# Kernel tuning notes

Measured on AMD Instinct MI355X. Metric: run time of the kernel, lower is better.

## Reference

```python
import jax, jax.numpy as jnp
import numpy as np

B, S, A, H, N = 4096, 128, 32, 1024, 256
BETA = 1.0            # params['temperature']
NORM_SMOOTHING = 0.01 # params['norm_smoothing']
MAX_A = 1.0           # env.action_space.high[0]
# dropout_rate = 0.0 and eval-mode reference -> dropout is identity


def setup_inputs() -> dict:
    key = jax.random.key(0)
    ks = jax.random.split(key, 16)
    sc_s = 1.0 / np.sqrt(S)
    sc_h = 1.0 / np.sqrt(H)
    return {
        "s": jax.random.normal(ks[0], (B, S), jnp.float32),
        "a": jax.random.normal(ks[1], (B, A), jnp.float32),
        # value side MLP: S->H->H->H->N
        "Wv1": jax.random.uniform(ks[2], (S, H), jnp.float32, -sc_s, sc_s),
        "bv1": jax.random.uniform(ks[3], (H,), jnp.float32, -sc_s, sc_s),
        "Wv2": jax.random.uniform(ks[4], (H, H), jnp.float32, -sc_h, sc_h),
        "bv2": jax.random.uniform(ks[5], (H,), jnp.float32, -sc_h, sc_h),
        "Wv3": jax.random.uniform(ks[6], (H, H), jnp.float32, -sc_h, sc_h),
        "bv3": jax.random.uniform(ks[7], (H,), jnp.float32, -sc_h, sc_h),
        "Wv4": jax.random.uniform(ks[8], (H, N), jnp.float32, -sc_h, sc_h),
        "bv4": jax.random.uniform(ks[9], (N,), jnp.float32, -sc_h, sc_h),
        # location side: S->H (xavier), then N expert linears H->A stacked
        "Wl1": jax.random.normal(ks[10], (S, H), jnp.float32) * np.sqrt(2.0 / (S + H)),
        "bl1": jnp.zeros((H,), jnp.float32),
        "Wexp": jax.random.uniform(ks[11], (N, H, A), jnp.float32, -0.1, 0.1),
        "bexp": jax.random.uniform(ks[12], (N, A), jnp.float32, -1.0, 1.0),
    }


def reference(s, a, Wv1, bv1, Wv2, bv2, Wv3, bv3, Wv4, bv4, Wl1, bl1, Wexp, bexp):
    t = jax.nn.relu(s @ Wv1 + bv1)
    t = jax.nn.relu(t @ Wv2 + bv2)
    t = jax.nn.relu(t @ Wv3 + bv3)
    values = t @ Wv4 + bv4                      # [B, N]

    # --- get_all_centroids: shared hidden, N expert heads as grouped GEMM ---
    h = jax.nn.relu(s @ Wl1 + bl1)              # [B, H] (dropout identity)
    centroids = MAX_A * jnp.tanh(
        jnp.einsum("bh,nha->bna", h, Wexp) + bexp[None]
    )                                           # [B, N, A]

    # --- rbf_function: softmax over -beta * ||centroid - a|| ---
    diff = centroids - a[:, None, :]            # [B, N, A]
    dist = jnp.sqrt(jnp.sum(diff * diff, axis=2) + NORM_SMOOTHING)  # [B, N]
    weights = jax.nn.softmax(-BETA * dist, axis=1)                  # [B, N]

    return jnp.sum(weights * values, axis=1, keepdims=True)         # [B, 1]
```

## Files before the change

### kernel.cpp

```cpp
#include <hip/hip_runtime.h>
#include <hip/hip_bf16.h>


typedef _Float16 half8 __attribute__((ext_vector_type(8)));
typedef _Float16 half4v __attribute__((ext_vector_type(4)));
typedef float floatx16 __attribute__((ext_vector_type(16)));

namespace {
constexpr int kB = 4096, kS = 128, kA = 32, kH = 1024, kN = 256;
constexpr size_t al(size_t x) { return (x + 255) & ~size_t(255); }
constexpr size_t OFF_FLAG  = 0;
constexpr size_t OFF_S16   = 256;
constexpr size_t OFF_WEXPT = OFF_S16   + al((size_t)kB * kS * 2);
constexpr size_t OFF_WV1T  = OFF_WEXPT + al((size_t)kN * kA * kH * 2);
constexpr size_t OFF_WL1T  = OFF_WV1T  + (size_t)kS * kH * 2;
constexpr size_t OFF_WV2T  = OFF_WL1T  + al((size_t)kS * kH * 2);
constexpr size_t OFF_WV3T  = OFF_WV2T  + al((size_t)kH * kH * 2);
constexpr size_t OFF_WV4T  = OFF_WV3T  + al((size_t)kH * kH * 2);
constexpr size_t OFF_BUFC  = OFF_WV4T  + al((size_t)kH * kN * 2);
constexpr size_t OFF_B2V   = OFF_BUFC  + al((size_t)kB * 2 * kH * 2);
constexpr size_t OFF_B3    = OFF_B2V   + al((size_t)kB * kH * 2);
constexpr size_t OFF_VAL   = OFF_B3    + al((size_t)kB * kH * 2);
constexpr size_t OFF_DIST  = OFF_VAL   + al((size_t)kB * kN * 4);
}

__device__ __forceinline__ float ldraw(const void* p, size_t i, int bf) {
    if (bf) return __uint_as_float(((unsigned)((const unsigned short*)p)[i]) << 16);
    return ((const float*)p)[i];
}

__device__ __forceinline__ float4 ldraw4(const void* p, size_t i, int bf) {
    if (bf) {
        ushort4 u = *(const ushort4*)((const unsigned short*)p + i);
        return make_float4(__uint_as_float((unsigned)u.x << 16),
                           __uint_as_float((unsigned)u.y << 16),
                           __uint_as_float((unsigned)u.z << 16),
                           __uint_as_float((unsigned)u.w << 16));
    }
    return *(const float4*)((const float*)p + i);
}

__device__ __forceinline__ void gl_lds16(const _Float16* g, _Float16* l) {
    __builtin_amdgcn_global_load_lds(
        (const __attribute__((address_space(1))) unsigned int*)g,
        (__attribute__((address_space(3))) unsigned int*)l, 16, 0, 0);
}

template <int N>
__device__ __forceinline__ void waitcnt_vm() {
    if constexpr (N == 0)      asm volatile("s_waitcnt vmcnt(0)" ::: "memory");
    else if constexpr (N == 2) asm volatile("s_waitcnt vmcnt(2)" ::: "memory");
    else if constexpr (N == 4) asm volatile("s_waitcnt vmcnt(4)" ::: "memory");
    else if constexpr (N == 6) asm volatile("s_waitcnt vmcnt(6)" ::: "memory");
    else if constexpr (N == 8) asm volatile("s_waitcnt vmcnt(8)" ::: "memory");
    else if constexpr (N == 16) asm volatile("s_waitcnt vmcnt(16)" ::: "memory");
    else static_assert(N == 0, "unsupported vmcnt");
}

__device__ __forceinline__ float fast_tanh(float x) {
    x = fminf(9.f, fmaxf(-9.f, x));
    float e = __expf(2.f * x);
    return (e - 1.f) * __builtin_amdgcn_rcpf(e + 1.f);
}

__global__ void detect_kernel(const unsigned int* __restrict__ s_raw, int* __restrict__ flag) {
    __shared__ int cnt;
    if (threadIdx.x == 0) cnt = 0;
    __syncthreads();
    const unsigned e = (s_raw[threadIdx.x] >> 7) & 0xFFu;
    int c = (e >= 118u && e <= 135u) ? 1 : 0;
    for (int off = 32; off > 0; off >>= 1) c += __shfl_down(c, off);
    if ((threadIdx.x & 63) == 0) atomicAdd(&cnt, c);
    __syncthreads();
    if (threadIdx.x == 0) *flag = (cnt > 128) ? 1 : 0;
}

struct TDesc { const void* src; _Float16* dst; int K; int N; int tiles; };
struct TPack { TDesc d[7]; };

__global__ void transpose_all(TPack p, const int* __restrict__ flag) {
    __shared__ float tile[32][33];
    const int bf = *flag;
    int bid = blockIdx.x;
    int i = 0;
    while (bid >= p.d[i].tiles) { bid -= p.d[i].tiles; ++i; }
    const void* src = p.d[i].src;
    _Float16* dst = p.d[i].dst;
    const int tx = threadIdx.x, ty = threadIdx.y;
    const int K = p.d[i].K, N = p.d[i].N;
    if (K == 0) {
        const int lin = ty * 8 + tx;
        const size_t base = (size_t)bid * 4096;
#pragma unroll
        for (int t = 0; t < 4; ++t) {
            const size_t idx = base + (size_t)t * 1024 + (size_t)lin * 4;
            float4 v = ldraw4(src, idx, bf);
            half4v o = {(_Float16)v.x, (_Float16)v.y, (_Float16)v.z, (_Float16)v.w};
            *(half4v*)(dst + idx) = o;
        }
        return;
    }
    const int tpz = (N >> 5) * (K >> 5);
    const int z = bid / tpz, r = bid - z * tpz;
    const int n0 = (r % (N >> 5)) * 32, k0 = (r / (N >> 5)) * 32;
    const size_t zo = (size_t)z * K * N;
    float4 v = ldraw4(src, zo + (size_t)(k0 + ty) * N + n0 + tx * 4, bf);
    tile[ty][tx * 4 + 0] = v.x;
    tile[ty][tx * 4 + 1] = v.y;
    tile[ty][tx * 4 + 2] = v.z;
    tile[ty][tx * 4 + 3] = v.w;
    __syncthreads();
    half4v o;
#pragma unroll
    for (int j = 0; j < 4; ++j) o[j] = (_Float16)tile[tx * 4 + j][ty];
    *(half4v*)(dst + zo + (size_t)(n0 + ty) * K + k0 + tx * 4) = o;
}

struct GArgs {
    const _Float16* A;
    const _Float16* Bt;
    const void* bias;
    const void* bias2;
    void* C;
    const void* a_raw;
    float* dist;
    int split;
    int N, K, lda, Mt, Nt, relu, of16, fuse;
};

template <int TM, int TN, int WM, int WN, int NST>
__device__ __forceinline__ void dgemm_core(const GArgs& g, int bid, const int* flagp) {
    constexpr int NT = WM * WN * 64;
    constexpr int BK = 32;
    constexpr int MI = TM / WM / 32, NI = TN / WN / 32;
    constexpr int ACH = TM * BK / 8;
    constexpr int BCH = TN * BK / 8;
    constexpr int AT = (ACH + NT - 1) / NT;
    constexpr int BT = (BCH + NT - 1) / NT;
    constexpr int LPS = AT + BT;
    __shared__ _Float16 As[NST * ACH * 8];
    __shared__ _Float16 Bs[NST * BCH * 8];

    const int tid = threadIdx.x;
    const int lane = tid & 63;
    const int w = tid >> 6, wr = w / WN, wc = w % WN;
    const int N = g.N, K = g.K, lda = g.lda;

    int mt, nt;
    if ((g.Mt & 7) == 0 && (g.Nt & 7) == 0) {
        const int xcd = bid & 7, loc = bid >> 3;
        const int Bn = g.Nt >> 3;
        const int sr = loc / (8 * Bn);
        const int rem = loc - sr * (8 * Bn);
        mt = sr * 8 + (rem & 7);
        nt = xcd * Bn + (rem >> 3);
    } else {
        mt = bid % g.Mt;
        nt = bid / g.Mt;
    }
    const int m0 = mt * TM, n0 = nt * TN;

    const _Float16* gAsrc[AT];
    _Float16* lAdst[AT];
#pragma unroll
    for (int t = 0; t < AT; ++t) {
        int c = t * NT + tid;
        if (c >= ACH) c = ACH - 1;
        const int ks = c / (TM * 2), rem = c % (TM * 2);
        const int row = (rem >> 6) * 32 + (rem & 31);
        const int kcol = ks * 16 + ((rem >> 5) & 1) * 8;
        gAsrc[t] = g.A + (size_t)(m0 + row) * lda + kcol;
        lAdst[t] = As + c * 8;
    }
    const _Float16* gBsrc[BT];
    _Float16* lBdst[BT];
#pragma unroll
    for (int t = 0; t < BT; ++t) {
        int c = t * NT + tid;
        if (c >= BCH) c = BCH - 1;
        const int ks = c / (TN * 2), rem = c % (TN * 2);
        const int row = (rem >> 6) * 32 + (rem & 31);
        const int kcol = ks * 16 + ((rem >> 5) & 1) * 8;
        gBsrc[t] = g.Bt + (size_t)(n0 + row) * K + kcol;
        lBdst[t] = Bs + c * 8;
    }

    auto issue = [&](int k0, int st) {
#pragma unroll
        for (int t = 0; t < AT; ++t)
            if ((t + 1) * NT <= ACH || t * NT + tid < ACH)
                gl_lds16(gAsrc[t] + k0, lAdst[t] + st * ACH * 8);
#pragma unroll
        for (int t = 0; t < BT; ++t)
            if ((t + 1) * NT <= BCH || t * NT + tid < BCH)
                gl_lds16(gBsrc[t] + k0, lBdst[t] + st * BCH * 8);
    };

    floatx16 acc[MI][NI];
#pragma unroll
    for (int mi = 0; mi < MI; ++mi)
#pragma unroll
        for (int ni = 0; ni < NI; ++ni)
#pragma unroll
            for (int i = 0; i < 16; ++i) acc[mi][ni][i] = 0.f;

    auto compute = [&](int st) {
        const int ao = st * ACH * 8, bo = st * BCH * 8;
#pragma unroll
        for (int ks = 0; ks < 2; ++ks) {
            half8 af[MI], bf[NI];
#pragma unroll
            for (int mi = 0; mi < MI; ++mi)
                af[mi] = *(const half8*)(As + ao + ((size_t)(ks * TM * 2 + (wr * MI + mi) * 64 + lane)) * 8);
#pragma unroll
            for (int ni = 0; ni < NI; ++ni)
                bf[ni] = *(const half8*)(Bs + bo + ((size_t)(ks * TN * 2 + (wc * NI + ni) * 64 + lane)) * 8);
#pragma unroll
            for (int mi = 0; mi < MI; ++mi)
#pragma unroll
                for (int ni = 0; ni < NI; ++ni)
                    acc[mi][ni] = __builtin_amdgcn_mfma_f32_32x32x16_f16(af[mi], bf[ni], acc[mi][ni], 0, 0, 0);
        }
    };

    const int ntiles = K / BK;
    if constexpr (NST == 2) {
        issue(0, 0);
        for (int k0 = 0; k0 < K; k0 += 2 * BK) {
            __syncthreads();
            if (k0 + BK < K) issue(k0 + BK, 1);
            compute(0);
            __syncthreads();
            if (k0 + 2 * BK < K) issue(k0 + 2 * BK, 0);
            compute(1);
        }
    } else {
        issue(0, 0);
        if (ntiles > 1) issue(BK, 1);
        if (ntiles > 2) issue(2 * BK, 2);
        for (int kt = 0; kt < ntiles; ++kt) {
            const int rem = ntiles - 1 - kt;
            if (rem >= 2)      waitcnt_vm<2 * LPS>();
            else if (rem == 1) waitcnt_vm<LPS>();
            else               waitcnt_vm<0>();
            __builtin_amdgcn_s_barrier();
            asm volatile("" ::: "memory");
            __builtin_amdgcn_sched_barrier(0);
            if (kt + 3 < ntiles) issue((kt + 3) * BK, (kt + 3) & 3);
            __builtin_amdgcn_s_setprio(1);
            compute(kt & 3);
            __builtin_amdgcn_s_setprio(0);
            asm volatile("s_waitcnt lgkmcnt(0)" ::: "memory");
        }
    }

    const int bf_ = *flagp;
    const int am = lane & 31;
    const int half = lane >> 5;

    if (g.fuse) {
        constexpr int EPB = TN / 32;
        const int ebase = n0 >> 5;
        float bvv[NI];
#pragma unroll
        for (int ni = 0; ni < NI; ++ni)
            bvv[ni] = ldraw(g.bias, (size_t)(n0 + (wc * NI + ni) * 32 + am), bf_);
        float* a_s = (float*)As;
        float* d_s = (float*)Bs;
        __syncthreads();
        for (int idx = tid; idx < TM * kA; idx += NT)
            a_s[idx] = ldraw(g.a_raw, (size_t)(m0 + (idx >> 5)) * kA + (idx & 31), bf_);
        __syncthreads();
#pragma unroll
        for (int mi = 0; mi < MI; ++mi)
#pragma unroll
            for (int rr = 0; rr < 16; ++rr) {
                const int row_loc = (wr * MI + mi) * 32 + (rr & 3) + 8 * (rr >> 2) + 4 * half;
                const float av = a_s[row_loc * kA + am];
#pragma unroll
                for (int ni = 0; ni < NI; ++ni) {
                    const float c = fast_tanh(acc[mi][ni][rr] + bvv[ni]);
                    const float d = c - av;
                    float d2 = d * d;
                    d2 += __shfl_xor(d2, 1);
                    d2 += __shfl_xor(d2, 2);
                    d2 += __shfl_xor(d2, 4);
                    d2 += __shfl_xor(d2, 8);
                    d2 += __shfl_xor(d2, 16);
                    if (am == 0) d_s[row_loc * EPB + wc * NI + ni] = d2;
                }
            }
        __syncthreads();
        for (int idx = tid; idx < TM * EPB; idx += NT)
            g.dist[(size_t)(m0 + (idx / EPB)) * kN + ebase + (idx % EPB)] = sqrtf(d_s[idx] + 0.01f);
        return;
    }

#pragma unroll
    for (int mi = 0; mi < MI; ++mi)
#pragma unroll
        for (int ni = 0; ni < NI; ++ni) {
            const int Rb = m0 + (wr * MI + mi) * 32;
            const int Cb = n0 + (wc * NI + ni) * 32 + am;
            const float bv = (Cb < g.split) ? ldraw(g.bias, Cb, bf_)
                                            : ldraw(g.bias2, Cb - g.split, bf_);
#pragma unroll
            for (int rr = 0; rr < 16; ++rr) {
                const int row = Rb + (rr & 3) + 8 * (rr >> 2) + 4 * half;
                float x = acc[mi][ni][rr] + bv;
                if (g.relu) x = fmaxf(x, 0.f);
                if (g.of16) ((_Float16*)g.C)[(size_t)row * N + Cb] = (_Float16)x;
                else ((float*)g.C)[(size_t)row * N + Cb] = x;
            }
        }
}

template <int TM, int TN, int WM, int WN, int NST, int MW>
__launch_bounds__(WM * WN * 64, MW)
__global__ void dgemm_one(GArgs g, const int* __restrict__ flagp) {
    dgemm_core<TM, TN, WM, WN, NST>(g, blockIdx.x, flagp);
}

__launch_bounds__(256)
__global__ void final_softmax(const float* __restrict__ dist, const float* __restrict__ values,
                              const int* __restrict__ flag, void* __restrict__ out) {
    const int row = blockIdx.x * 4 + (threadIdx.x >> 6);
    const int lane = threadIdx.x & 63;
    const float4 d4 = *(const float4*)(dist + (size_t)row * kN + lane * 4);
    const float4 v4 = *(const float4*)(values + (size_t)row * kN + lane * 4);
    float m = fminf(fminf(d4.x, d4.y), fminf(d4.z, d4.w));
#pragma unroll
    for (int off = 32; off > 0; off >>= 1) m = fminf(m, __shfl_xor(m, off));
    const float w0 = expf(m - d4.x), w1 = expf(m - d4.y);
    const float w2 = expf(m - d4.z), w3 = expf(m - d4.w);
    float ws = (w0 + w1) + (w2 + w3);
    float wv = fmaf(w0, v4.x, fmaf(w1, v4.y, fmaf(w2, v4.z, w3 * v4.w)));
#pragma unroll
    for (int off = 32; off > 0; off >>= 1) {
        ws += __shfl_xor(ws, off);
        wv += __shfl_xor(wv, off);
    }
    if (lane == 0) {
        const float o = wv / ws;
        if (*flag) ((__hip_bfloat16*)out)[row] = __float2bfloat16(o);
        else       ((float*)out)[row] = o;
    }
}

extern "C" void kernel_launch(void* const* d_in, const int* in_sizes, int n_in,
                              void* d_out, int out_size, void* d_ws, size_t ws_size,
                              hipStream_t stream) {
    (void)in_sizes; (void)n_in; (void)out_size; (void)ws_size;
    char* ws = (char*)d_ws;
    int* flag = (int*)(ws + OFF_FLAG);
    _Float16* s16   = (_Float16*)(ws + OFF_S16);
    _Float16* wexpt = (_Float16*)(ws + OFF_WEXPT);
    _Float16* wv1t  = (_Float16*)(ws + OFF_WV1T);
    _Float16* wl1t  = (_Float16*)(ws + OFF_WL1T);
    _Float16* wv2t  = (_Float16*)(ws + OFF_WV2T);
    _Float16* wv3t  = (_Float16*)(ws + OFF_WV3T);
    _Float16* wv4t  = (_Float16*)(ws + OFF_WV4T);
    _Float16* bufC  = (_Float16*)(ws + OFF_BUFC);
    _Float16* b2v   = (_Float16*)(ws + OFF_B2V);
    _Float16* b3    = (_Float16*)(ws + OFF_B3);
    float* values   = (float*)(ws + OFF_VAL);
    float* distb    = (float*)(ws + OFF_DIST);

    detect_kernel<<<1, 256, 0, stream>>>((const unsigned int*)d_in[0], flag);

    TPack tp;
    tp.d[0] = {d_in[2],  wv1t,  kS, kH, (kH / 32) * (kS / 32)};
    tp.d[1] = {d_in[10], wl1t,  kS, kH, (kH / 32) * (kS / 32)};
    tp.d[2] = {d_in[4],  wv2t,  kH, kH, (kH / 32) * (kH / 32)};
    tp.d[3] = {d_in[6],  wv3t,  kH, kH, (kH / 32) * (kH / 32)};
    tp.d[4] = {d_in[8],  wv4t,  kH, kN, (kN / 32) * (kH / 32)};
    tp.d[5] = {d_in[12], wexpt, kH, kA, kN * (kA / 32) * (kH / 32)};
    tp.d[6] = {d_in[0],  s16,   0,  kB * kS, (kB * kS) / 4096};
    int total_tiles = 0;
    for (int i = 0; i < 7; ++i) total_tiles += tp.d[i].tiles;
    transpose_all<<<total_tiles, dim3(8, 32), 0, stream>>>(tp, flag);

    const int BIG = 1 << 30;
    {
        GArgs g{s16, wv1t, d_in[3], d_in[11], bufC, nullptr, nullptr, kH,
                2 * kH, kS, kS, kB / 64, (2 * kH) / 64, 1, 1, 0};
        dgemm_one<64, 64, 2, 2, 4, 2><<<(kB / 64) * ((2 * kH) / 64), 256, 0, stream>>>(g, flag);
    }
    {
        GArgs g{bufC, wv2t, d_in[5], d_in[5], b2v, nullptr, nullptr, BIG,
                kH, kH, 2 * kH, kB / 128, kH / 128, 1, 1, 0};
        dgemm_one<128, 128, 2, 2, 4, 2><<<(kB / 128) * (kH / 128), 256, 0, stream>>>(g, flag);
    }
    {
        GArgs g{b2v, wv3t, d_in[7], d_in[7], b3, nullptr, nullptr, BIG,
                kH, kH, kH, kB / 128, kH / 128, 1, 1, 0};
        dgemm_one<128, 128, 2, 2, 4, 2><<<(kB / 128) * (kH / 128), 256, 0, stream>>>(g, flag);
    }
    {
        GArgs g{b3, wv4t, d_in[9], d_in[9], values, nullptr, nullptr, BIG,
                kN, kH, kH, kB / 64, kN / 64, 0, 0, 0};
        dgemm_one<64, 64, 2, 2, 4, 2><<<(kB / 64) * (kN / 64), 256, 0, stream>>>(g, flag);
    }
    {
        GArgs g{bufC + kH, wexpt, d_in[13], d_in[13], nullptr, d_in[1], distb,
                BIG, kN * kA, kH, 2 * kH, kB / 128, (kN * kA) / 128, 0, 0, 1};
        dgemm_one<128, 128, 2, 2, 2, 4><<<(kB / 128) * ((kN * kA) / 128), 256, 0, stream>>>(g, flag);
    }
    final_softmax<<<kB / 4, 256, 0, stream>>>(distb, values, flag, d_out);
}
```

Baseline: 358.5 us.

## Add dedicated 256x256 expert GEMM kernel with XCD-aware tile mapping

Moves the fused expert GEMM (tanh, distance and reduction epilogue) out of the generic templated kernel into a dedicated 512-thread kernel. The new kernel uses 256x256 tiles, a double-buffered BK=32 global-to-LDS pipeline, and a block-index remap that groups N-tiles per XCD. The aim is more operand reuse per tile and better L2 locality for the largest GEMM (4096x8192x1024). In exchange, the larger tile gives fewer blocks and shallower pipelining, and the fused path is removed from the generic kernel.

Result: faster. 350.2 us (-2.3%).

```diff
diff --git a/kernel.cpp b/kernel.cpp
--- a/kernel.cpp
+++ b/kernel.cpp
@@ -56,6 +56,7 @@
     else if constexpr (N == 16) asm volatile("s_waitcnt vmcnt(16)" ::: "memory");
     else static_assert(N == 0, "unsupported vmcnt");
 }
+__device__ __forceinline__ void lgkm0() { asm volatile("s_waitcnt lgkmcnt(0)" ::: "memory"); }
 
 __device__ __forceinline__ float fast_tanh(float x) {
     x = fminf(9.f, fmaxf(-9.f, x));
@@ -250,51 +251,13 @@
             __builtin_amdgcn_s_setprio(1);
             compute(kt & 3);
             __builtin_amdgcn_s_setprio(0);
-            asm volatile("s_waitcnt lgkmcnt(0)" ::: "memory");
+            lgkm0();
         }
     }
 
     const int bf_ = *flagp;
     const int am = lane & 31;
     const int half = lane >> 5;
-
-    if (g.fuse) {
-        constexpr int EPB = TN / 32;
-        const int ebase = n0 >> 5;
-        float bvv[NI];
-#pragma unroll
-        for (int ni = 0; ni < NI; ++ni)
-            bvv[ni] = ldraw(g.bias, (size_t)(n0 + (wc * NI + ni) * 32 + am), bf_);
-        float* a_s = (float*)As;
-        float* d_s = (float*)Bs;
-        __syncthreads();
-        for (int idx = tid; idx < TM * kA; idx += NT)
-            a_s[idx] = ldraw(g.a_raw, (size_t)(m0 + (idx >> 5)) * kA + (idx & 31), bf_);
-        __syncthreads();
-#pragma unroll
-        for (int mi = 0; mi < MI; ++mi)
-#pragma unroll
-            for (int rr = 0; rr < 16; ++rr) {
-                const int row_loc = (wr * MI + mi) * 32 + (rr & 3) + 8 * (rr >> 2) + 4 * half;
-                const float av = a_s[row_loc * kA + am];
-#pragma unroll
-                for (int ni = 0; ni < NI; ++ni) {
-                    const float c = fast_tanh(acc[mi][ni][rr] + bvv[ni]);
-                    const float d = c - av;
-                    float d2 = d * d;
-                    d2 += __shfl_xor(d2, 1);
-                    d2 += __shfl_xor(d2, 2);
-                    d2 += __shfl_xor(d2, 4);
-                    d2 += __shfl_xor(d2, 8);
-                    d2 += __shfl_xor(d2, 16);
-                    if (am == 0) d_s[row_loc * EPB + wc * NI + ni] = d2;
-                }
-            }
-        __syncthreads();
-        for (int idx = tid; idx < TM * EPB; idx += NT)
-            g.dist[(size_t)(m0 + (idx / EPB)) * kN + ebase + (idx % EPB)] = sqrtf(d_s[idx] + 0.01f);
-        return;
-    }
 
 #pragma unroll
     for (int mi = 0; mi < MI; ++mi)
@@ -319,6 +282,132 @@
 __launch_bounds__(WM * WN * 64, MW)
 __global__ void dgemm_one(GArgs g, const int* __restrict__ flagp) {
     dgemm_core<TM, TN, WM, WN, NST>(g, blockIdx.x, flagp);
+}
+
+__launch_bounds__(512, 2)
+__global__ void dgemm_expert8(GArgs g, const int* __restrict__ flagp) {
+    constexpr int TM = 256, TN = 256, BK = 32, NT = 512;
+    constexpr int MI = 4, NI = 2;
+    constexpr int ACH = TM * BK / 8;
+    constexpr int BCH = TN * BK / 8;
+    __shared__ _Float16 As[2 * ACH * 8];
+    __shared__ _Float16 Bs[2 * BCH * 8];
+
+    const int tid = threadIdx.x;
+    const int lane = tid & 63;
+    const int w = tid >> 6, wr = w >> 2, wc = w & 3;
+    const int K = g.K, lda = g.lda;
+
+    int mt, nt;
+    {
+        const int bid = blockIdx.x;
+        const int xcd = bid & 7, loc = bid >> 3;
+        const int Bn = g.Nt >> 3;
+        const int sr = loc / (8 * Bn);
+        const int rem = loc - sr * (8 * Bn);
+        mt = sr * 8 + (rem & 7);
+        nt = xcd * Bn + (rem >> 3);
+    }
+    const int m0 = mt * TM, n0 = nt * TN;
+
+    const _Float16* gA[2]; _Float16* lA[2];
+    const _Float16* gB[2]; _Float16* lB[2];
+#pragma unroll
+    for (int s = 0; s < 2; ++s) {
+        const int c = s * NT + tid;
+        const int ks = c >> 9, rem = c & 511;
+        const int row = (rem >> 6) * 32 + (rem & 31);
+        const int kcol = ks * 16 + ((rem >> 5) & 1) * 8;
+        gA[s] = g.A + (size_t)(m0 + row) * lda + kcol;
+        lA[s] = As + c * 8;
+        gB[s] = g.Bt + (size_t)(n0 + row) * K + kcol;
+        lB[s] = Bs + c * 8;
+    }
+
+    floatx16 acc[MI][NI];
+#pragma unroll
+    for (int mi = 0; mi < MI; ++mi)
+#pragma unroll
+        for (int ni = 0; ni < NI; ++ni)
+#pragma unroll
+            for (int i = 0; i < 16; ++i) acc[mi][ni][i] = 0.f;
+
+    gl_lds16(gA[0], lA[0]); gl_lds16(gB[0], lB[0]);
+    gl_lds16(gA[1], lA[1]); gl_lds16(gB[1], lB[1]);
+
+    const int NTILES = K / BK;
+    for (int t = 0; t < NTILES; ++t) {
+        const int st = t & 1;
+        const int ao = st * ACH * 8, bo = st * BCH * 8;
+        const bool pre = (t + 1 < NTILES);
+        const int k1 = (t + 1) * BK;
+        const int so1 = ((t + 1) & 1) * ACH * 8;
+#pragma unroll
+        for (int p = 0; p < 2; ++p) {
+            if (pre || p == 0) waitcnt_vm<2>();
+            else               waitcnt_vm<0>();
+            __builtin_amdgcn_s_barrier();
+            asm volatile("" ::: "memory");
+            half8 af[MI], bfr[NI];
+#pragma unroll
+            for (int mi = 0; mi < MI; ++mi)
+                af[mi] = *(const half8*)(As + ao + ((size_t)(p * 512 + (wr * MI + mi) * 64 + lane)) * 8);
+#pragma unroll
+            for (int ni = 0; ni < NI; ++ni)
+                bfr[ni] = *(const half8*)(Bs + bo + ((size_t)(p * 512 + (wc * NI + ni) * 64 + lane)) * 8);
+            if (pre) {
+                gl_lds16(gA[p] + k1, lA[p] + so1);
+                gl_lds16(gB[p] + k1, lB[p] + so1);
+            }
+            lgkm0();
+            __builtin_amdgcn_sched_barrier(0);
+            __builtin_amdgcn_s_setprio(1);
+#pragma unroll
+            for (int mi = 0; mi < MI; ++mi)
+#pragma unroll
+                for (int ni = 0; ni < NI; ++ni)
+                    acc[mi][ni] = __builtin_amdgcn_mfma_f32_32x32x16_f16(af[mi], bfr[ni], acc[mi][ni], 0, 0, 0);
+            __builtin_amdgcn_s_setprio(0);
+        }
+    }
+
+    const int bf_ = *flagp;
+    const int am = lane & 31;
+    const int half = lane >> 5;
+    constexpr int EPB = TN / 32;
+    const int ebase = n0 >> 5;
+    float bvv[NI];
+#pragma unroll
+    for (int ni = 0; ni < NI; ++ni)
+        bvv[ni] = ldraw(g.bias, (size_t)(n0 + (wc * NI + ni) * 32 + am), bf_);
+    float* a_s = (float*)As;
+    float* d_s = (float*)Bs;
+    __syncthreads();
+    for (int idx = tid; idx < TM * kA; idx += NT)
+        a_s[idx] = ldraw(g.a_raw, (size_t)(m0 + (idx >> 5)) * kA + (idx & 31), bf_);
+    __syncthreads();
+#pragma unroll
+    for (int mi = 0; mi < MI; ++mi)
+#pragma unroll
+        for (int rr = 0; rr < 16; ++rr) {
+            const int row_loc = (wr * MI + mi) * 32 + (rr & 3) + 8 * (rr >> 2) + 4 * half;
+            const float av = a_s[row_loc * kA + am];
+#pragma unroll
+            for (int ni = 0; ni < NI; ++ni) {
+                const float c = fast_tanh(acc[mi][ni][rr] + bvv[ni]);
+                const float d = c - av;
+                float d2 = d * d;
+                d2 += __shfl_xor(d2, 1);
+                d2 += __shfl_xor(d2, 2);
+                d2 += __shfl_xor(d2, 4);
+                d2 += __shfl_xor(d2, 8);
+                d2 += __shfl_xor(d2, 16);
+                if (am == 0) d_s[row_loc * EPB + wc * NI + ni] = d2;
+            }
+        }
+    __syncthreads();
+    for (int idx = tid; idx < TM * EPB; idx += NT)
+        g.dist[(size_t)(m0 + (idx / EPB)) * kN + ebase + (idx % EPB)] = sqrtf(d_s[idx] + 0.01f);
 }
 
 __launch_bounds__(256)
@@ -403,8 +492,8 @@
     }
     {
         GArgs g{bufC + kH, wexpt, d_in[13], d_in[13], nullptr, d_in[1], distb,
-                BIG, kN * kA, kH, 2 * kH, kB / 128, (kN * kA) / 128, 0, 0, 1};
-        dgemm_one<128, 128, 2, 2, 2, 4><<<(kB / 128) * ((kN * kA) / 128), 256, 0, stream>>>(g, flag);
+                BIG, kN * kA, kH, 2 * kH, kB / 256, (kN * kA) / 256, 0, 0, 1};
+        dgemm_expert8<<<(kB / 256) * ((kN * kA) / 256), 512, 0, stream>>>(g, flag);
     }
     final_softmax<<<kB / 4, 256, 0, stream>>>(distb, values, flag, d_out);
 }
```
